# Kernel tuning notes

Measured on AMD Instinct MI355X. Metric: run time of the kernel, lower is better.

## Reference

```python
import jax, jax.numpy as jnp
import numpy as np
import math

B, N, E = 32, 512, 8192          # graphs, nodes/graph, edges/graph
IN_DIM, D, H, HD, L, C = 64, 128, 4, 32, 3, 10
HID = 2 * D                      # _FeatureMLP hidden = max(d, 2*d)


def _ln(x, g, b, eps=1e-5):
    mu = x.mean(-1, keepdims=True)
    var = ((x - mu) ** 2).mean(-1, keepdims=True)
    return (x - mu) / jnp.sqrt(var + eps) * g + b


def _gelu(x):
    return jax.nn.gelu(x, approximate=False)  # torch nn.GELU default (erf)


def setup_inputs() -> dict:
    key = jax.random.key(0)
    ks = iter(jax.random.split(key, 48))
    def w(*shape):
        return jax.random.normal(next(ks), shape, jnp.float32) * 0.02
    z = lambda *s: jnp.zeros(s, jnp.float32)
    o = lambda *s: jnp.ones(s, jnp.float32)
    return {
        'x': jax.random.normal(next(ks), (B * N, IN_DIM), jnp.float32),
        'src': jax.random.randint(next(ks), (B, E), 0, N),
        'dst': jax.random.randint(next(ks), (B, E), 0, N),
        # node encoder: Linear -> LN -> GELU -> Linear -> LN
        'enc_w1': w(IN_DIM, HID), 'enc_b1': z(HID), 'enc_g1': o(HID), 'enc_bn1': z(HID),
        'enc_w2': w(HID, D), 'enc_b2': z(D), 'enc_g2': o(D), 'enc_bn2': z(D),
        # per-layer edge-message MLP (stacked over L)
        'msg_w1': w(L, 2 * D, D), 'msg_b1': z(L, D),
        'msg_w2': w(L, D, D), 'msg_b2': z(L, D),
        'msg_g': o(L, D), 'msg_bb': z(L, D),
        # per-layer attention
        'qw': w(L, D, H * HD), 'qb': z(L, H * HD),
        'kw': w(L, D, H * HD), 'kb': z(L, H * HD),
        'vw': w(L, D, H * HD), 'vb': z(L, H * HD),
        'ow': w(L, H * HD, D), 'ob': z(L, D),
        'attn_g': o(L, D), 'attn_b': z(L, D),
        # graph head: Linear(4d,2d) -> GELU -> LN -> Linear(2d,C)
        'gh_w1': w(4 * D, 2 * D), 'gh_b1': z(2 * D),
        'gh_g': o(2 * D), 'gh_bn': z(2 * D),
        'gh_w2': w(2 * D, C), 'gh_b2': z(C),
    }


def reference(x, src, dst, enc_w1, enc_b1, enc_g1, enc_bn1, enc_w2, enc_b2, enc_g2, enc_bn2,
              msg_w1, msg_b1, msg_w2, msg_b2, msg_g, msg_bb,
              qw, qb, kw, kb, vw, vb, ow, ob, attn_g, attn_b,
              gh_w1, gh_b1, gh_g, gh_bn, gh_w2, gh_b2):
    # node encoder
    t = _ln(x @ enc_w1 + enc_b1, enc_g1, enc_bn1)
    h = _ln(_gelu(t) @ enc_w2 + enc_b2, enc_g2, enc_bn2)
    h = h.reshape(B, N, D)
    seg = jax.vmap(lambda m, d: jax.ops.segment_sum(m, d, num_segments=N))
    for l in range(L):
        # edge message block: gather src/dst, MLP, scatter-add to dst
        hs = jnp.take_along_axis(h, src[..., None], axis=1)   # [B,E,D]
        hd = jnp.take_along_axis(h, dst[..., None], axis=1)   # [B,E,D]
        m = _gelu(jnp.concatenate([hs, hd], -1) @ msg_w1[l] + msg_b1[l]) @ msg_w2[l] + msg_b2[l]
        h = _ln(h + seg(m, dst), msg_g[l], msg_bb[l])
        # masked attention block (dense per-graph attention)
        q = (h @ qw[l] + qb[l]).reshape(B, N, H, HD)
        k = (h @ kw[l] + kb[l]).reshape(B, N, H, HD)
        v = (h @ vw[l] + vb[l]).reshape(B, N, H, HD)
        scores = jnp.einsum('bnhd,bmhd->bhnm', q, k) / math.sqrt(HD)
        attn = jax.nn.softmax(scores, axis=-1)
        o = jnp.einsum('bhnm,bmhd->bnhd', attn, v).reshape(B, N, H * HD)
        h = _ln(h + o @ ow[l] + ob[l], attn_g[l], attn_b[l])
    # graph pooling: mean | sum | max | std
    mean = h.mean(1)
    summ = h.sum(1)
    mx = h.max(1)
    std = jnp.sqrt(jax.nn.relu((h ** 2).mean(1) - mean ** 2) + 1e-6)
    pool = jnp.concatenate([mean, summ, mx, std], -1)         # [B,4D]
    g = _ln(_gelu(pool @ gh_w1 + gh_b1), gh_g, gh_bn)
    return g @ gh_w2 + gh_b2                                   # [B,C]
```

## Files before the change

kernel.cpp:

```cpp
#include <hip/hip_runtime.h>
#include <cmath>

#define B_   32
#define N_   512
#define E_   8192
#define BN_  16384
#define D_   128

typedef short bf16x8 __attribute__((ext_vector_type(8)));
typedef float f32x4  __attribute__((ext_vector_type(4)));

static __device__ __forceinline__ float bf2f(unsigned short u){
  union{unsigned int i; float f;} v; v.i = ((unsigned int)u)<<16; return v.f;
}
static __device__ __forceinline__ unsigned short f2bf(float f){
  union{unsigned int i; float f;} v; v.f=f;
  unsigned int x=v.i;
  return (unsigned short)((x + 0x7fffu + ((x>>16)&1u))>>16);
}
static __device__ __forceinline__ unsigned int pack2(float a, float b){
  return (unsigned int)f2bf(a) | ((unsigned int)f2bf(b)<<16);
}
static __device__ __forceinline__ float gelu_f(float x){
  float xs=x*0.70710678118654752f;
  float ax=fabsf(xs);
  float t=__builtin_amdgcn_rcpf(1.0f+0.3275911f*ax);
  float p=t*(0.254829592f+t*(-0.284496736f+t*(1.421413741f+t*(-1.453152027f+t*1.061405429f))));
  float er=1.0f - p*__expf(-ax*ax);
  er = (xs<0.f)? -er : er;
  return 0.5f*x*(1.0f+er);
}
static __device__ __forceinline__ float gelu_t(float x){
  float x2=x*x;
  float y=x*(-1.5957691216f + x2*(-0.0713548162f));
  float e=__expf(y);
  return x*__builtin_amdgcn_rcpf(1.0f+e);
}
static __device__ __forceinline__ float ldin(const void* p, size_t i, int isbf){
  return isbf ? bf2f(((const unsigned short*)p)[i]) : ((const float*)p)[i];
}

static __device__ __forceinline__ void block_sum2(float a, float b, float&A, float&Bv, float* red, int nw){
  int lane=threadIdx.x&63, w=threadIdx.x>>6;
  #pragma unroll
  for(int o=32;o>0;o>>=1){ a+=__shfl_down(a,o); b+=__shfl_down(b,o); }
  if(lane==0){ red[w]=a; red[8+w]=b; }
  __syncthreads();
  float sa=0.f, sb=0.f;
  for(int i=0;i<nw;i++){ sa+=red[i]; sb+=red[8+i]; }
  __syncthreads();
  A=sa; Bv=sb;
}

__global__ void sniff_kernel(const unsigned int* __restrict__ xw, int* __restrict__ flag){
  int t=threadIdx.x;
  int cnt=0;
  for(int i=0;i<32;i++){
    unsigned int w=xw[t+64*i];
    float v=bf2f((unsigned short)(w&0xffffu));
    float av=fabsf(v);
    if(v==0.0f || (av>=6e-5f && av<=8.0f)) cnt++;
  }
  #pragma unroll
  for(int o=32;o>0;o>>=1) cnt+=__shfl_down(cnt,o);
  if(t==0) *flag=(cnt>=1024)?1:0;
}

__global__ __launch_bounds__(256) void count_kernel(
  const int* __restrict__ dst, int* __restrict__ cnt)
{
  __shared__ int lc[512];
  int g=blockIdx.x, c=blockIdx.y, t=threadIdx.x;
  for(int i=t;i<512;i+=256) lc[i]=0;
  __syncthreads();
  for(int e=t;e<1024;e+=256) atomicAdd(&lc[dst[(size_t)g*E_+c*1024+e]],1);
  __syncthreads();
  for(int i=t;i<512;i+=256){ int v=lc[i]; if(v) atomicAdd(&cnt[g*512+i],v); }
}

__global__ __launch_bounds__(256) void scan_kernel(
  int* __restrict__ cnt, int* __restrict__ rowptr)
{
  __shared__ int sc[512];
  int g=blockIdx.x, t=threadIdx.x;
  for(int i=t;i<512;i+=256) sc[i]=cnt[g*512+i];
  __syncthreads();
  if(t==0){
    int acc=0;
    for(int i=0;i<512;i++){ int c=sc[i]; rowptr[g*513+i]=acc; cnt[g*512+i]=acc; acc+=c; }
    rowptr[g*513+512]=acc;
  }
}

__global__ __launch_bounds__(256) void scatter_kernel(
  const int* __restrict__ src, const int* __restrict__ dst,
  int* __restrict__ off, unsigned short* __restrict__ ss)
{
  int g=blockIdx.x, c=blockIdx.y, t=threadIdx.x;
  for(int e=t;e<1024;e+=256){
    size_t idx=(size_t)g*E_+c*1024+e;
    int d=dst[idx];
    int pos=atomicAdd(&off[g*512+d],1);
    ss[(size_t)g*E_+pos]=(unsigned short)src[idx];
  }
}

__global__ __launch_bounds__(256) void prep_kernel(
  const void* __restrict__ msg_w1, const void* __restrict__ msg_w2,
  const void* __restrict__ qw, const void* __restrict__ kw,
  const void* __restrict__ vw, const void* __restrict__ ow,
  const void* __restrict__ qb, const void* __restrict__ kb, const void* __restrict__ vb,
  const void* __restrict__ ob, const void* __restrict__ msg_b1, const void* __restrict__ msg_b2,
  const void* __restrict__ msg_g, const void* __restrict__ msg_bb,
  const void* __restrict__ attn_g, const void* __restrict__ attn_b,
  const void* __restrict__ enc_w1, const void* __restrict__ enc_w2,
  const void* __restrict__ enc_b1, const void* __restrict__ enc_g1, const void* __restrict__ enc_bn1,
  const void* __restrict__ enc_b2, const void* __restrict__ enc_g2, const void* __restrict__ enc_bn2,
  const void* __restrict__ gh_w1, const void* __restrict__ gh_w2,
  const void* __restrict__ gh_b1, const void* __restrict__ gh_g,
  const void* __restrict__ gh_bn, const void* __restrict__ gh_b2,
  unsigned short* __restrict__ w1t, unsigned short* __restrict__ w2k,
  unsigned short* __restrict__ qkvt, unsigned short* __restrict__ owt,
  unsigned short* __restrict__ w1te, unsigned short* __restrict__ w2te,
  unsigned short* __restrict__ ghw1t, unsigned short* __restrict__ ghw2t,
  unsigned short* __restrict__ cb, const int* __restrict__ flag)
{
  int isbf=*flag;
  int job=blockIdx.y;
  int i=blockIdx.x*256+threadIdx.x;
  if(job<3){
    if(i<32768){ int l=job; int k=i>>7, n=i&127; w1t[l*32768 + n*256 + k]=f2bf(ldin(msg_w1,(size_t)l*32768+i,isbf)); }
  } else if(job<6){
    int l=job-3; if(i<16384){ w2k[l*16384 + i]=f2bf(ldin(msg_w2,(size_t)l*16384+i,isbf)); }
  } else if(job<15){
    int r=job-6, l=r/3, which=r%3;
    if(i<16384){ int k=i>>7, n=i&127;
      const void* w=(which==0)?qw:((which==1)?kw:vw);
      qkvt[l*49152 + (which*128+n)*128 + k]=f2bf(ldin(w,(size_t)l*16384+i,isbf)); }
  } else if(job<18){
    int l=job-15; if(i<16384){ int k=i>>7, n=i&127; owt[l*16384 + n*128 + k]=f2bf(ldin(ow,(size_t)l*16384+i,isbf)); }
  } else if(job==18){
    if(i<3840){
      float v;
      if(i<1152){ int l=i/384, j=i%384, which=j>>7, jj=j&127;
        const void* bb=(which==0)?qb:((which==1)?kb:vb);
        v=ldin(bb,(size_t)l*128+jj,isbf);
      } else {
        int i2=i-1152; int r=i2/384; int rem=i2%384;
        const void* s = (r==0)?ob:((r==1)?msg_b1:((r==2)?msg_b2:((r==3)?msg_g:((r==4)?msg_bb:((r==5)?attn_g:attn_b)))));
        v=ldin(s,(size_t)rem,isbf);
      }
      cb[i]=f2bf(v);
    }
  } else if(job==19){
    if(i<1152){
      float v;
      if(i<256)       v=ldin(enc_b1,i,isbf);
      else if(i<512)  v=ldin(enc_g1,i-256,isbf);
      else if(i<768)  v=ldin(enc_bn1,i-512,isbf);
      else if(i<896)  v=ldin(enc_b2,i-768,isbf);
      else if(i<1024) v=ldin(enc_g2,i-896,isbf);
      else            v=ldin(enc_bn2,i-1024,isbf);
      cb[3840+i]=f2bf(v);
    }
  } else if(job==20){
    if(i<16384){ int k=i>>8, n=i&255; w1te[n*64+k]=f2bf(ldin(enc_w1,(size_t)i,isbf)); }
  } else if(job==21){
    if(i<32768){ int k=i>>7, n=i&127; w2te[n*256+k]=f2bf(ldin(enc_w2,(size_t)i,isbf)); }
  } else if(job<26){
    int p=job-22; int j=p*32768+i;
    if(i<32768){ int k=j>>8, n=j&255; ghw1t[n*512+k]=f2bf(ldin(gh_w1,(size_t)j,isbf)); }
  } else {
    if(i<2560){ int k=i/10, n=i%10; ghw2t[n*256+k]=f2bf(ldin(gh_w2,(size_t)i,isbf)); }
    else if(i<2560+778){
      int j=i-2560; float v;
      if(j<256)      v=ldin(gh_b1,j,isbf);
      else if(j<512) v=ldin(gh_g,j-256,isbf);
      else if(j<768) v=ldin(gh_bn,j-512,isbf);
      else           v=ldin(gh_b2,j-768,isbf);
      cb[4992+j]=f2bf(v);
    }
  }
}

__global__ __launch_bounds__(256) void enc_kernel(
  const void* __restrict__ x, const unsigned short* __restrict__ w1te,
  const unsigned short* __restrict__ w2te, const unsigned short* __restrict__ cb,
  unsigned short* __restrict__ h, const int* __restrict__ flag)
{
  __shared__ __align__(16) unsigned short xs[64][72];
  __shared__ __align__(16) unsigned short t1[64][264];
  int isbf=*flag;
  int m0=blockIdx.x*64;
  int t=threadIdx.x, lane=t&63, w=t>>6, quad=lane>>4, ln=lane&15;
  for(int c2=t;c2<1024;c2+=256){
    int i=c2*4, row=i>>6, col=i&63;
    float v0,v1,v2,v3;
    if(isbf){
      const unsigned short* p=(const unsigned short*)x+(size_t)m0*64+i;
      v0=bf2f(p[0]); v1=bf2f(p[1]); v2=bf2f(p[2]); v3=bf2f(p[3]);
    } else {
      float4 f=*(const float4*)((const float*)x+(size_t)m0*64+i);
      v0=f.x; v1=f.y; v2=f.z; v3=f.w;
    }
    ushort4 o; o.x=f2bf(v0); o.y=f2bf(v1); o.z=f2bf(v2); o.w=f2bf(v3);
    *(ushort4*)&xs[row][col]=o;
  }
  __syncthreads();
  f32x4 a[4][4];
  #pragma unroll
  for(int nt=0;nt<4;nt++){ a[nt][0]={0,0,0,0}; a[nt][1]={0,0,0,0}; a[nt][2]={0,0,0,0}; a[nt][3]={0,0,0,0}; }
  #pragma unroll
  for(int k0i=0;k0i<2;k0i++){
    bf16x8 af[4];
    #pragma unroll
    for(int f=0;f<4;f++) af[f]=*(const bf16x8*)(&xs[f*16+ln][k0i*32+quad*8]);
    #pragma unroll
    for(int nt=0;nt<4;nt++){
      int n=w*64+nt*16+ln;
      bf16x8 bfr=*(const bf16x8*)(w1te+(size_t)n*64+k0i*32+quad*8);
      #pragma unroll
      for(int f=0;f<4;f++) a[nt][f]=__builtin_amdgcn_mfma_f32_16x16x32_bf16(af[f],bfr,a[nt][f],0,0,0);
    }
  }
  #pragma unroll
  for(int nt=0;nt<4;nt++){
    int n=w*64+nt*16+ln;
    float bv=bf2f(cb[3840+n]);
    #pragma unroll
    for(int f=0;f<4;f++)
      #pragma unroll
      for(int r=0;r<4;r++) t1[f*16+quad*4+r][n]=f2bf(a[nt][f][r]+bv);
  }
  __syncthreads();
  {
    int row=t>>2, qq=t&3;
    float s=0.f,s2=0.f;
    for(int c=qq*64;c<qq*64+64;c++){ float v=bf2f(t1[row][c]); s+=v; s2+=v*v; }
    s+=__shfl_xor(s,1); s+=__shfl_xor(s,2);
    s2+=__shfl_xor(s2,1); s2+=__shfl_xor(s2,2);
    float mu=s*(1.f/256.f), var=fmaxf(s2*(1.f/256.f)-mu*mu,0.f);
    float rr=rsqrtf(var+1e-5f);
    for(int c=qq*64;c<qq*64+64;c++){
      float v=bf2f(t1[row][c]);
      t1[row][c]=f2bf(gelu_f((v-mu)*rr*bf2f(cb[4096+c])+bf2f(cb[4352+c])));
    }
  }
  __syncthreads();
  f32x4 b2a[2][4];
  #pragma unroll
  for(int nt=0;nt<2;nt++){ b2a[nt][0]={0,0,0,0}; b2a[nt][1]={0,0,0,0}; b2a[nt][2]={0,0,0,0}; b2a[nt][3]={0,0,0,0}; }
  #pragma unroll
  for(int k0i=0;k0i<8;k0i++){
    bf16x8 af[4];
    #pragma unroll
    for(int f=0;f<4;f++) af[f]=*(const bf16x8*)(&t1[f*16+ln][k0i*32+quad*8]);
    #pragma unroll
    for(int nt=0;nt<2;nt++){
      int n=w*32+nt*16+ln;
      bf16x8 bfr=*(const bf16x8*)(w2te+(size_t)n*256+k0i*32+quad*8);
      #pragma unroll
      for(int f=0;f<4;f++) b2a[nt][f]=__builtin_amdgcn_mfma_f32_16x16x32_bf16(af[f],bfr,b2a[nt][f],0,0,0);
    }
  }
  __syncthreads();
  float* mf=(float*)&t1[0][0];
  #pragma unroll
  for(int nt=0;nt<2;nt++){
    int n=w*32+nt*16+ln;
    float bv=bf2f(cb[4608+n]);
    #pragma unroll
    for(int f=0;f<4;f++)
      #pragma unroll
      for(int r=0;r<4;r++) mf[(f*16+quad*4+r)*132+n]=b2a[nt][f][r]+bv;
  }
  __syncthreads();
  {
    int row=t>>2, qq=t&3;
    float s=0.f,s2=0.f;
    for(int c=qq*32;c<qq*32+32;c++){ float v=mf[row*132+c]; s+=v; s2+=v*v; }
    s+=__shfl_xor(s,1); s+=__shfl_xor(s,2);
    s2+=__shfl_xor(s2,1); s2+=__shfl_xor(s2,2);
    float mu=s*(1.f/128.f), var=fmaxf(s2*(1.f/128.f)-mu*mu,0.f);
    float rr=rsqrtf(var+1e-5f);
    for(int c=qq*32;c<qq*32+32;c+=2){
      float v0=(mf[row*132+c  ]-mu)*rr*bf2f(cb[4736+c  ])+bf2f(cb[4864+c  ]);
      float v1=(mf[row*132+c+1]-mu)*rr*bf2f(cb[4736+c+1])+bf2f(cb[4864+c+1]);
      *(unsigned int*)(h+(size_t)(m0+row)*128+c)=pack2(v0,v1);
    }
  }
}

__global__ __launch_bounds__(256) void uvgen_kernel(
  const unsigned short* __restrict__ hrows, const unsigned short* __restrict__ w1t,
  const unsigned short* __restrict__ b1, unsigned short* __restrict__ UV)
{
  __shared__ __align__(16) unsigned short a_t[64][136];
  int t=threadIdx.x;
  int m0=blockIdx.x*64;
  int y=blockIdx.y;
  for(int c=t;c<1024;c+=256){
    int m=c>>4, pp=c&15;
    *(uint4*)&a_t[m][pp*8]=*((const uint4*)(hrows+(size_t)(m0+m)*128)+pp);
  }
  __syncthreads();
  int lane=t&63, w=t>>6, quad=lane>>4, ln=lane&15;
  #pragma unroll
  for(int nt=0;nt<2;nt++){
    int n=w*32+nt*16+ln;
    f32x4 a0={0,0,0,0},a1={0,0,0,0},a2={0,0,0,0},a3={0,0,0,0};
    const unsigned short* wp=w1t+(size_t)n*256+y*128+quad*8;
    #pragma unroll
    for(int k0=0;k0<128;k0+=32){
      bf16x8 bfr=*(const bf16x8*)(wp+k0);
      bf16x8 f0=*(const bf16x8*)(&a_t[ln   ][k0+quad*8]);
      bf16x8 f1=*(const bf16x8*)(&a_t[16+ln][k0+quad*8]);
      bf16x8 f2=*(const bf16x8*)(&a_t[32+ln][k0+quad*8]);
      bf16x8 f3=*(const bf16x8*)(&a_t[48+ln][k0+quad*8]);
      a0=__builtin_amdgcn_mfma_f32_16x16x32_bf16(f0,bfr,a0,0,0,0);
      a1=__builtin_amdgcn_mfma_f32_16x16x32_bf16(f1,bfr,a1,0,0,0);
      a2=__builtin_amdgcn_mfma_f32_16x16x32_bf16(f2,bfr,a2,0,0,0);
      a3=__builtin_amdgcn_mfma_f32_16x16x32_bf16(f3,bfr,a3,0,0,0);
    }
    float bv=y?0.f:bf2f(b1[n]);
    #pragma unroll
    for(int r2=0;r2<4;r2++){
      UV[(size_t)(m0+quad*4+r2   )*256+y*128+n]=f2bf(a0[r2]+bv);
      UV[(size_t)(m0+16+quad*4+r2)*256+y*128+n]=f2bf(a1[r2]+bv);
      UV[(size_t)(m0+32+quad*4+r2)*256+y*128+n]=f2bf(a2[r2]+bv);
      UV[(size_t)(m0+48+quad*4+r2)*256+y*128+n]=f2bf(a3[r2]+bv);
    }
  }
}

__global__ __launch_bounds__(128) void edgef_kernel(
  unsigned short* __restrict__ h,
  const unsigned short* __restrict__ UV,
  const unsigned short* __restrict__ ss,
  const int* __restrict__ rowptr,
  const unsigned short* __restrict__ w2k,
  const unsigned short* __restrict__ b2,
  const unsigned short* __restrict__ gg, const unsigned short* __restrict__ bbp,
  int b0, int gEp)
{
  __shared__ __align__(16) float aggL[2][4][128];
  __shared__ __align__(16) float po[2][4][128];
  int t=threadIdx.x, lane=t&63, w=t>>6;
  int bid=blockIdx.x;
  int lg=bid%gEp, ch=bid/gEp;
  int g=b0+lg;
  const unsigned short* UVg = UV + (size_t)lg*512*256;
  const unsigned short* ssg = ss + (size_t)g*E_;
  int dbase = ch*4;
  int bnd[5];
  #pragma unroll
  for(int i=0;i<5;i++) bnd[i]=rowptr[g*513+dbase+i];
  #pragma unroll 1
  for(int dd=0;dd<4;dd++){
    int e_lo=bnd[dd], e_hi0=bnd[dd+1];
    int half=(e_hi0-e_lo+1)>>1;
    int es = w ? (e_lo+half) : e_lo;
    int ee = w ? e_hi0       : (e_lo+half);
    unsigned int vdw=*(const unsigned int*)(UVg + (size_t)(dbase+dd)*256 + 128 + lane*2);
    float v0=bf2f((unsigned short)(vdw&0xffffu)), v1=bf2f((unsigned short)(vdw>>16));
    float a0=0.f, a1=0.f;
    int si3,si4,si5;
    unsigned int u0,u1,u2;
    {
      int s0=__builtin_amdgcn_readfirstlane((int)ssg[es  ])&511;
      int s1=__builtin_amdgcn_readfirstlane((int)ssg[es+1])&511;
      int s2=__builtin_amdgcn_readfirstlane((int)ssg[es+2])&511;
      si3=(int)ssg[es+3]; si4=(int)ssg[es+4]; si5=(int)ssg[es+5];
      u0=*(const unsigned int*)(UVg + (size_t)s0*256 + lane*2);
      u1=*(const unsigned int*)(UVg + (size_t)s1*256 + lane*2);
      u2=*(const unsigned int*)(UVg + (size_t)s2*256 + lane*2);
    }
    #pragma unroll 2
    for(int e=es;e<ee;e++){
      float z0=bf2f((unsigned short)(u0&0xffffu))+v0;
      float z1=bf2f((unsigned short)(u0>>16))+v1;
      u0=u1; u1=u2;
      int s3=__builtin_amdgcn_readfirstlane(si3)&511;
      u2=*(const unsigned int*)(UVg + (size_t)s3*256 + lane*2);
      si3=si4; si4=si5;
      si5=(int)ssg[e+6];
      a0+=gelu_t(z0); a1+=gelu_t(z1);
    }
    aggL[w][dd][lane*2  ]=a0;
    aggL[w][dd][lane*2+1]=a1;
  }
  __syncthreads();
  float o[4][2];
  #pragma unroll
  for(int dd=0;dd<4;dd++){ o[dd][0]=0.f; o[dd][1]=0.f; }
  #pragma unroll 4
  for(int kk=0;kk<64;kk++){
    int k=w*64+kk;
    unsigned int wdw=*(const unsigned int*)(w2k+(size_t)k*128+lane*2);
    float w0=bf2f((unsigned short)(wdw&0xffffu));
    float w1=bf2f((unsigned short)(wdw>>16));
    #pragma unroll
    for(int dd=0;dd<4;dd++){
      float av=aggL[0][dd][k]+aggL[1][dd][k];
      o[dd][0]+=av*w0; o[dd][1]+=av*w1;
    }
  }
  #pragma unroll
  for(int dd=0;dd<4;dd++){
    po[w][dd][lane*2  ]=o[dd][0];
    po[w][dd][lane*2+1]=o[dd][1];
  }
  __syncthreads();
  #pragma unroll 1
  for(int p=0;p<2;p++){
    int di=w*2+p;
    int d = dbase + di;
    float deg=(float)(bnd[di+1]-bnd[di]);
    float o0=bf2f(b2[lane*2  ])*deg + po[0][di][lane*2  ] + po[1][di][lane*2  ];
    float o1=bf2f(b2[lane*2+1])*deg + po[0][di][lane*2+1] + po[1][di][lane*2+1];
    size_t base=(size_t)(g*512+d)*128;
    unsigned int hdw=*(const unsigned int*)(h+base+lane*2);
    float x0=bf2f((unsigned short)(hdw&0xffffu))+o0;
    float x1=bf2f((unsigned short)(hdw>>16))+o1;
    float s1=x0+x1, s2=x0*x0+x1*x1;
    #pragma unroll
    for(int off=32;off>0;off>>=1){ s1+=__shfl_xor(s1,off); s2+=__shfl_xor(s2,off); }
    float mu=s1*(1.f/128.f), var=fmaxf(s2*(1.f/128.f)-mu*mu,0.f);
    float rr=rsqrtf(var+1e-5f);
    float y0=(x0-mu)*rr*bf2f(gg[lane*2  ])+bf2f(bbp[lane*2  ]);
    float y1=(x1-mu)*rr*bf2f(gg[lane*2+1])+bf2f(bbp[lane*2+1]);
    *(unsigned int*)(h+base+lane*2)=pack2(y0,y1);
  }
}

__global__ __launch_bounds__(256) void attnf_kernel(
  const unsigned short* __restrict__ h, const unsigned short* __restrict__ wqkv,
  const unsigned short* __restrict__ bq, unsigned short* __restrict__ obuf, int b0, int gA)
{
  __shared__ __align__(16) unsigned short Qs[128][40];
  __shared__ __align__(16) unsigned short Ks[64][72];
  __shared__ __align__(16) unsigned short Vts[32][72];
  __shared__ __align__(16) unsigned short Ps[64][72];
  int bx=blockIdx.x;
  int lg=bx%gA; int rr2=bx/gA; int hh=rr2&3, qq4=rr2>>2;
  int g=b0+lg;
  int t=threadIdx.x, lane=t&63, w=t>>6, quad=lane>>4, ln=lane&15;
  const unsigned short* hg=h+(size_t)g*512*128;
  const float sc=0.17677669529663689f;
  bf16x8 wk[2][4], wv[2][4];
  #pragma unroll
  for(int nt=0;nt<2;nt++)
    #pragma unroll
    for(int k0i=0;k0i<4;k0i++){
      int n=hh*32+nt*16+ln;
      wk[nt][k0i]=*(const bf16x8*)(wqkv+(size_t)(128+n)*128+k0i*32+quad*8);
      wv[nt][k0i]=*(const bf16x8*)(wqkv+(size_t)(256+n)*128+k0i*32+quad*8);
    }
  #pragma unroll
  for(int qt=0;qt<2;qt++){
    int r0=qq4*128+qt*64+w*16;
    bf16x8 af[4];
    #pragma unroll
    for(int k0i=0;k0i<4;k0i++) af[k0i]=*(const bf16x8*)(hg+(size_t)(r0+ln)*128+k0i*32+quad*8);
    #pragma unroll
    for(int nt=0;nt<2;nt++){
      int dim=nt*16+ln;
      f32x4 c={0,0,0,0};
      #pragma unroll
      for(int k0i=0;k0i<4;k0i++){
        bf16x8 bfr=*(const bf16x8*)(wqkv+(size_t)(hh*32+dim)*128+k0i*32+quad*8);
        c=__builtin_amdgcn_mfma_f32_16x16x32_bf16(af[k0i],bfr,c,0,0,0);
      }
      float bv=bf2f(bq[hh*32+dim]);
      #pragma unroll
      for(int r=0;r<4;r++) Qs[qt*64+w*16+quad*4+r][dim]=f2bf((c[r]+bv)*sc);
    }
  }
  f32x4 O[2][2]; float Lp[2][4];
  #pragma unroll
  for(int qt=0;qt<2;qt++){ O[qt][0]={0,0,0,0}; O[qt][1]={0,0,0,0};
    #pragma unroll
    for(int r=0;r<4;r++) Lp[qt][r]=0.f; }
  for(int kc=0;kc<8;kc++){
    __syncthreads();
    {
      int r0=kc*64+w*16;
      bf16x8 af[4];
      #pragma unroll
      for(int k0i=0;k0i<4;k0i++) af[k0i]=*(const bf16x8*)(hg+(size_t)(r0+ln)*128+k0i*32+quad*8);
      #pragma unroll
      for(int nt=0;nt<2;nt++){
        int dim=nt*16+ln;
        f32x4 ck={0,0,0,0}, cv={0,0,0,0};
        #pragma unroll
        for(int k0i=0;k0i<4;k0i++){
          ck=__builtin_amdgcn_mfma_f32_16x16x32_bf16(af[k0i],wk[nt][k0i],ck,0,0,0);
          cv=__builtin_amdgcn_mfma_f32_16x16x32_bf16(af[k0i],wv[nt][k0i],cv,0,0,0);
        }
        float bk=bf2f(bq[128+hh*32+dim]), bv2=bf2f(bq[256+hh*32+dim]);
        #pragma unroll
        for(int r=0;r<4;r++){
          int key=w*16+quad*4+r;
          Ks[key][dim]=f2bf(ck[r]+bk);
          Vts[dim][key]=f2bf(cv[r]+bv2);
        }
      }
    }
    __syncthreads();
    #pragma unroll
    for(int qt=0;qt<2;qt++){
      bf16x8 qf=*(const bf16x8*)(&Qs[qt*64+w*16+ln][quad*8]);
      f32x4 s[4];
      #pragma unroll
      for(int f=0;f<4;f++){
        bf16x8 kf=*(const bf16x8*)(&Ks[f*16+ln][quad*8]);
        f32x4 z={0,0,0,0};
        s[f]=__builtin_amdgcn_mfma_f32_16x16x32_bf16(qf,kf,z,0,0,0);
      }
      #pragma unroll
      for(int f=0;f<4;f++)
        #pragma unroll
        for(int r=0;r<4;r++){
          float pe=__expf(fminf(s[f][r],30.0f));
          Ps[w*16+quad*4+r][f*16+ln]=f2bf(pe);
          Lp[qt][r]+=pe;
        }
      #pragma unroll
      for(int s2=0;s2<2;s2++){
        bf16x8 pf=*(const bf16x8*)(&Ps[w*16+ln][s2*32+quad*8]);
        bf16x8 v0=*(const bf16x8*)(&Vts[ln   ][s2*32+quad*8]);
        bf16x8 v1=*(const bf16x8*)(&Vts[16+ln][s2*32+quad*8]);
        O[qt][0]=__builtin_amdgcn_mfma_f32_16x16x32_bf16(pf,v0,O[qt][0],0,0,0);
        O[qt][1]=__builtin_amdgcn_mfma_f32_16x16x32_bf16(pf,v1,O[qt][1],0,0,0);
      }
    }
  }
  #pragma unroll
  for(int qt=0;qt<2;qt++){
    #pragma unroll
    for(int o=1;o<16;o<<=1)
      #pragma unroll
      for(int r=0;r<4;r++) Lp[qt][r]+=__shfl_xor(Lp[qt][r],o);
    #pragma unroll
    for(int r=0;r<4;r++){
      float inv=1.0f/Lp[qt][r];
      size_t row=(size_t)lg*512+qq4*128+qt*64+w*16+quad*4+r;
      obuf[row*128+hh*32+ln   ]=f2bf(O[qt][0][r]*inv);
      obuf[row*128+hh*32+16+ln]=f2bf(O[qt][1][r]*inv);
    }
  }
}

__global__ __launch_bounds__(256) void oproj_kernel(
  const unsigned short* __restrict__ obuf, const unsigned short* __restrict__ wo,
  const unsigned short* __restrict__ bo, unsigned short* __restrict__ h,
  const unsigned short* __restrict__ gg, const unsigned short* __restrict__ bbp, int b0)
{
  __shared__ __align__(16) unsigned short a_t[64][136];
  __shared__ float mf[64][132];
  int t=threadIdx.x, lane=t&63, w=t>>6, quad=lane>>4, ln=lane&15;
  int m0=blockIdx.x*64;
  for(int c=t;c<64*16;c+=256){
    int m=c>>4, pp=c&15;
    *(uint4*)&a_t[m][pp*8]=*((const uint4*)(obuf+(size_t)(m0+m)*128)+pp);
  }
  __syncthreads();
  #pragma unroll
  for(int nt=0;nt<2;nt++){
    int n=w*32+nt*16+ln;
    f32x4 a0={0,0,0,0},a1={0,0,0,0},a2={0,0,0,0},a3={0,0,0,0};
    const unsigned short* wp=wo+(size_t)n*128+quad*8;
    #pragma unroll
    for(int k0=0;k0<128;k0+=32){
      bf16x8 bfr=*(const bf16x8*)(wp+k0);
      bf16x8 f0=*(const bf16x8*)(&a_t[ln   ][k0+quad*8]);
      bf16x8 f1=*(const bf16x8*)(&a_t[16+ln][k0+quad*8]);
      bf16x8 f2=*(const bf16x8*)(&a_t[32+ln][k0+quad*8]);
      bf16x8 f3=*(const bf16x8*)(&a_t[48+ln][k0+quad*8]);
      a0=__builtin_amdgcn_mfma_f32_16x16x32_bf16(f0,bfr,a0,0,0,0);
      a1=__builtin_amdgcn_mfma_f32_16x16x32_bf16(f1,bfr,a1,0,0,0);
      a2=__builtin_amdgcn_mfma_f32_16x16x32_bf16(f2,bfr,a2,0,0,0);
      a3=__builtin_amdgcn_mfma_f32_16x16x32_bf16(f3,bfr,a3,0,0,0);
    }
    float bv=bf2f(bo[n]);
    #pragma unroll
    for(int r=0;r<4;r++){
      mf[quad*4+r   ][n]=a0[r]+bv;
      mf[16+quad*4+r][n]=a1[r]+bv;
      mf[32+quad*4+r][n]=a2[r]+bv;
      mf[48+quad*4+r][n]=a3[r]+bv;
    }
  }
  __syncthreads();
  {
    int row=t>>2, qq=t&3;
    size_t base=(size_t)(b0*512+m0+row)*128;
    float s=0.f,s2=0.f;
    float vals[32];
    for(int j=0;j<32;j++){
      int c=qq*32+j;
      float v=bf2f(h[base+c])+mf[row][c];
      vals[j]=v; s+=v; s2+=v*v;
    }
    s+=__shfl_xor(s,1); s+=__shfl_xor(s,2);
    s2+=__shfl_xor(s2,1); s2+=__shfl_xor(s2,2);
    float mu=s*(1.f/128.f), var=fmaxf(s2*(1.f/128.f)-mu*mu,0.f);
    float rr=rsqrtf(var+1e-5f);
    for(int j=0;j<32;j+=2){
      int c=qq*32+j;
      float v0=(vals[j]  -mu)*rr*bf2f(gg[c  ])+bf2f(bbp[c  ]);
      float v1=(vals[j+1]-mu)*rr*bf2f(gg[c+1])+bf2f(bbp[c+1]);
      *(unsigned int*)(h+base+c)=pack2(v0,v1);
    }
  }
}

__global__ __launch_bounds__(256) void poolp_kernel(
  const unsigned short* __restrict__ h, float* __restrict__ part)
{
  __shared__ float ps[256], ps2[256], pm[256];
  int b=blockIdx.x, c=blockIdx.y;
  int t=threadIdx.x, d=t&127, hf=t>>7;
  float s=0.f,s2=0.f,mx=-1e30f;
  for(int r=hf*32;r<hf*32+32;r++){
    float v=bf2f(h[((size_t)(b*512+c*64+r))*128+d]);
    s+=v; s2+=v*v; mx=fmaxf(mx,v);
  }
  ps[t]=s; ps2[t]=s2; pm[t]=mx;
  __syncthreads();
  if(t<128){
    s=ps[t]+ps[128+t]; s2=ps2[t]+ps2[128+t]; mx=fmaxf(pm[t],pm[128+t]);
    size_t base=((size_t)(b*8+c))*384;
    part[base+t]=s; part[base+128+t]=s2; part[base+256+t]=mx;
  }
}

__global__ __launch_bounds__(256) void head_kernel(
  const float* __restrict__ part, const unsigned short* __restrict__ ghw1t,
  const unsigned short* __restrict__ ghw2t, const unsigned short* __restrict__ cb,
  void* __restrict__ out, const int* __restrict__ flag)
{
  int isbf=*flag;
  int b=blockIdx.x, t=threadIdx.x;
  __shared__ float pl[512];
  __shared__ float gl[256];
  __shared__ float red[16];
  if(t<128){
    float s=0.f,s2=0.f,mx=-1e30f;
    for(int c=0;c<8;c++){
      size_t base=((size_t)(b*8+c))*384;
      s += part[base+t];
      s2+= part[base+128+t];
      mx = fmaxf(mx, part[base+256+t]);
    }
    float mean=s*(1.f/512.f);
    float var=fmaxf(s2*(1.f/512.f)-mean*mean,0.f);
    float sd=sqrtf(var+1e-6f);
    pl[t]=mean; pl[128+t]=s; pl[256+t]=mx; pl[384+t]=sd;
  }
  __syncthreads();
  float a=bf2f(cb[4992+t]);
  const unsigned short* wr=ghw1t+(size_t)t*512;
  for(int k0=0;k0<512;k0+=8){
    bf16x8 wv=*(const bf16x8*)(wr+k0);
    const unsigned short* wp=(const unsigned short*)&wv;
    #pragma unroll
    for(int j=0;j<8;j++) a+=pl[k0+j]*bf2f(wp[j]);
  }
  float u=gelu_f(a);
  float S,S2; block_sum2(u,u*u,S,S2,red,4);
  float mu=S*(1.f/256.f), var=fmaxf(S2*(1.f/256.f)-mu*mu,0.f);
  float r=rsqrtf(var+1e-5f);
  gl[t]=(u-mu)*r*bf2f(cb[5248+t])+bf2f(cb[5504+t]);
  __syncthreads();
  if(t<10){
    float o=bf2f(cb[5760+t]);
    const unsigned short* wr2=ghw2t+(size_t)t*256;
    for(int k0=0;k0<256;k0+=8){
      bf16x8 wv=*(const bf16x8*)(wr2+k0);
      const unsigned short* wp=(const unsigned short*)&wv;
      #pragma unroll
      for(int j=0;j<8;j++) o+=gl[k0+j]*bf2f(wp[j]);
    }
    if(isbf) ((unsigned short*)out)[b*10+t]=f2bf(o);
    else     ((float*)out)[b*10+t]=o;
  }
}

extern "C" void kernel_launch(void* const* d_in, const int* in_sizes, int n_in,
                              void* d_out, int out_size, void* d_ws, size_t ws_size,
                              hipStream_t stream)
{
  const void* x      =d_in[0];
  const int*  src    =(const int*)d_in[1];
  const int*  dstp   =(const int*)d_in[2];
  const void* enc_w1 =d_in[3];  const void* enc_b1 =d_in[4];
  const void* enc_g1 =d_in[5];  const void* enc_bn1=d_in[6];
  const void* enc_w2 =d_in[7];  const void* enc_b2 =d_in[8];
  const void* enc_g2 =d_in[9];  const void* enc_bn2=d_in[10];
  const void* msg_w1 =d_in[11]; const void* msg_b1 =d_in[12];
  const void* msg_w2 =d_in[13]; const void* msg_b2 =d_in[14];
  const void* msg_g  =d_in[15]; const void* msg_bb =d_in[16];
  const void* qw     =d_in[17]; const void* qb     =d_in[18];
  const void* kw     =d_in[19]; const void* kb     =d_in[20];
  const void* vw     =d_in[21]; const void* vb     =d_in[22];
  const void* ow     =d_in[23]; const void* ob     =d_in[24];
  const void* attn_g =d_in[25]; const void* attn_b =d_in[26];
  const void* gh_w1  =d_in[27]; const void* gh_b1  =d_in[28];
  const void* gh_g   =d_in[29]; const void* gh_bn  =d_in[30];
  const void* gh_w2  =d_in[31]; const void* gh_b2  =d_in[32];
  (void)in_sizes; (void)n_in; (void)out_size;

  const size_t MB=1024*1024;
  char* base=(char*)d_ws;
  unsigned short* h    =(unsigned short*)(base);
  unsigned short* w1t  =(unsigned short*)(base + 4194304);
  unsigned short* w2k  =(unsigned short*)(base + 4390912);
  unsigned short* qkvt =(unsigned short*)(base + 4489216);
  unsigned short* owt  =(unsigned short*)(base + 4784128);
  unsigned short* w1te =(unsigned short*)(base + 4882432);
  unsigned short* w2te =(unsigned short*)(base + 4915200);
  unsigned short* ghw1t=(unsigned short*)(base + 4980736);
  unsigned short* ghw2t=(unsigned short*)(base + 5242880);
  unsigned short* cb   =(unsigned short*)(base + 5248000);
  int*   rowptr        =(int*)(base + 5325312);
  int*   flag          =(int*)(base + 5390976);
  int*   cnt           =(int*)(base + 5391360);
  unsigned short* ssrt =(unsigned short*)(base + 5505024);
  char* R              = base + 6029312;

  int epass, apass;
  if(ws_size >= (size_t)(14.5*MB)){ epass=1; apass=1; }
  else if(ws_size >= 10*MB){ epass=2; apass=1; }
  else { epass=4; apass=2; }
  int gEp=B_/epass, gA=B_/apass;
  int rowsA=gA*512;
  float* part=(float*)R;

  sniff_kernel<<<1,64,0,stream>>>((const unsigned int*)x, flag);
  hipMemsetAsync(cnt,0,65536,stream);
  count_kernel<<<dim3(B_,8),256,0,stream>>>(dstp,cnt);
  scan_kernel<<<B_,256,0,stream>>>(cnt,rowptr);
  scatter_kernel<<<dim3(B_,8),256,0,stream>>>(src,dstp,cnt,ssrt);
  prep_kernel<<<dim3(128,27),256,0,stream>>>(msg_w1,msg_w2,qw,kw,vw,ow,qb,kb,vb,
      ob,msg_b1,msg_b2,msg_g,msg_bb,attn_g,attn_b,
      enc_w1,enc_w2,enc_b1,enc_g1,enc_bn1,enc_b2,enc_g2,enc_bn2,
      gh_w1,gh_w2,gh_b1,gh_g,gh_bn,gh_b2,
      w1t,w2k,qkvt,owt,w1te,w2te,ghw1t,ghw2t,cb,flag);

  enc_kernel<<<BN_/64,256,0,stream>>>(x,w1te,w2te,cb,h,flag);

  for(int l=0;l<3;l++){
    for(int ep=0;ep<epass;ep++){
      int b0=ep*gEp;
      unsigned short* UV=(unsigned short*)R;
      uvgen_kernel<<<dim3(gEp*8,2),256,0,stream>>>(h+(size_t)b0*512*128,
          w1t+(size_t)l*32768, cb+1536+l*128, UV);
      edgef_kernel<<<gEp*128,128,0,stream>>>(h,UV,ssrt,rowptr,
          w2k+(size_t)l*16384, cb+1920+l*128, cb+2304+l*128, cb+2688+l*128, b0, gEp);
    }
    for(int ap=0;ap<apass;ap++){
      int b0=ap*gA;
      unsigned short* obuf=(unsigned short*)R;
      attnf_kernel<<<gA*16,256,0,stream>>>(h, qkvt+(size_t)l*49152, cb+l*384, obuf, b0, gA);
      oproj_kernel<<<rowsA/64,256,0,stream>>>(obuf, owt+(size_t)l*16384,
          cb+1152+l*128, h, cb+3072+l*128, cb+3456+l*128, b0);
    }
  }
  poolp_kernel<<<dim3(B_,8),256,0,stream>>>(h,part);
  head_kernel<<<B_,256,0,stream>>>(part,ghw1t,ghw2t,cb,d_out,flag);
}
```

Baseline: 436.9 us.

## Precompute Q/K/V in separate GEMM kernel instead of recomputing inside attention

Adds a qkvgen kernel that computes Q (pre-scaled), K, and a transposed V for all nodes once per layer and writes them to workspace. The attention kernel then loads K and V fragments directly from global memory instead of recomputing the K/V projections in every block (each of the 4 query-tiles per head previously recomputed K/V for all 512 keys). This also removes the LDS staging and two barriers per key chunk. In exchange it adds a kernel launch and extra global traffic for Q/K/V, and the workspace split into passes now depends on available capacity.

```diff
diff --git a/kernel.cpp b/kernel.cpp
--- a/kernel.cpp
+++ b/kernel.cpp
@@ -333,6 +333,73 @@
   }
 }
 
+__global__ __launch_bounds__(256) void qkvgen_kernel(
+  const unsigned short* __restrict__ hrows, const unsigned short* __restrict__ wqkv,
+  const unsigned short* __restrict__ bqkv,
+  unsigned short* __restrict__ Qb, unsigned short* __restrict__ Kb,
+  unsigned short* __restrict__ Vtb)
+{
+  __shared__ __align__(16) unsigned short a_t[64][136];
+  int t=threadIdx.x;
+  int m0=blockIdx.x*64;
+  int y=blockIdx.y;
+  for(int c=t;c<1024;c+=256){
+    int m=c>>4, pp=c&15;
+    *(uint4*)&a_t[m][pp*8]=*((const uint4*)(hrows+(size_t)(m0+m)*128)+pp);
+  }
+  __syncthreads();
+  int lane=t&63, w=t>>6, quad=lane>>4, ln=lane&15;
+  int gloc=m0>>9, r0=m0&511;
+  #pragma unroll
+  for(int nt=0;nt<2;nt++){
+    int n=w*32+nt*16+ln;
+    f32x4 a0={0,0,0,0},a1={0,0,0,0},a2={0,0,0,0},a3={0,0,0,0};
+    const unsigned short* wp=wqkv+(size_t)(y*128+n)*128+quad*8;
+    #pragma unroll
+    for(int k0=0;k0<128;k0+=32){
+      bf16x8 bfr=*(const bf16x8*)(wp+k0);
+      bf16x8 f0=*(const bf16x8*)(&a_t[ln   ][k0+quad*8]);
+      bf16x8 f1=*(const bf16x8*)(&a_t[16+ln][k0+quad*8]);
+      bf16x8 f2=*(const bf16x8*)(&a_t[32+ln][k0+quad*8]);
+      bf16x8 f3=*(const bf16x8*)(&a_t[48+ln][k0+quad*8]);
+      a0=__builtin_amdgcn_mfma_f32_16x16x32_bf16(f0,bfr,a0,0,0,0);
+      a1=__builtin_amdgcn_mfma_f32_16x16x32_bf16(f1,bfr,a1,0,0,0);
+      a2=__builtin_amdgcn_mfma_f32_16x16x32_bf16(f2,bfr,a2,0,0,0);
+      a3=__builtin_amdgcn_mfma_f32_16x16x32_bf16(f3,bfr,a3,0,0,0);
+    }
+    float bv=bf2f(bqkv[y*128+n]);
+    if(y==0){
+      const float sc=0.17677669529663689f;
+      #pragma unroll
+      for(int r=0;r<4;r++){
+        Qb[(size_t)(m0   +quad*4+r)*128+n]=f2bf((a0[r]+bv)*sc);
+        Qb[(size_t)(m0+16+quad*4+r)*128+n]=f2bf((a1[r]+bv)*sc);
+        Qb[(size_t)(m0+32+quad*4+r)*128+n]=f2bf((a2[r]+bv)*sc);
+        Qb[(size_t)(m0+48+quad*4+r)*128+n]=f2bf((a3[r]+bv)*sc);
+      }
+    } else if(y==1){
+      #pragma unroll
+      for(int r=0;r<4;r++){
+        Kb[(size_t)(m0   +quad*4+r)*128+n]=f2bf(a0[r]+bv);
+        Kb[(size_t)(m0+16+quad*4+r)*128+n]=f2bf(a1[r]+bv);
+        Kb[(size_t)(m0+32+quad*4+r)*128+n]=f2bf(a2[r]+bv);
+        Kb[(size_t)(m0+48+quad*4+r)*128+n]=f2bf(a3[r]+bv);
+      }
+    } else {
+      unsigned short* vrow = Vtb + ((size_t)gloc*128+n)*512 + r0 + quad*4;
+      ushort4 o;
+      o.x=f2bf(a0[0]+bv); o.y=f2bf(a0[1]+bv); o.z=f2bf(a0[2]+bv); o.w=f2bf(a0[3]+bv);
+      *(ushort4*)(vrow)=o;
+      o.x=f2bf(a1[0]+bv); o.y=f2bf(a1[1]+bv); o.z=f2bf(a1[2]+bv); o.w=f2bf(a1[3]+bv);
+      *(ushort4*)(vrow+16)=o;
+      o.x=f2bf(a2[0]+bv); o.y=f2bf(a2[1]+bv); o.z=f2bf(a2[2]+bv); o.w=f2bf(a2[3]+bv);
+      *(ushort4*)(vrow+32)=o;
+      o.x=f2bf(a3[0]+bv); o.y=f2bf(a3[1]+bv); o.z=f2bf(a3[2]+bv); o.w=f2bf(a3[3]+bv);
+      *(ushort4*)(vrow+48)=o;
+    }
+  }
+}
+
 __global__ __launch_bounds__(128) void edgef_kernel(
   unsigned short* __restrict__ h,
   const unsigned short* __restrict__ UV,
@@ -434,88 +501,41 @@
 }
 
 __global__ __launch_bounds__(256) void attnf_kernel(
-  const unsigned short* __restrict__ h, const unsigned short* __restrict__ wqkv,
-  const unsigned short* __restrict__ bq, unsigned short* __restrict__ obuf, int b0, int gA)
-{
-  __shared__ __align__(16) unsigned short Qs[128][40];
-  __shared__ __align__(16) unsigned short Ks[64][72];
-  __shared__ __align__(16) unsigned short Vts[32][72];
+  const unsigned short* __restrict__ Qb, const unsigned short* __restrict__ Kb,
+  const unsigned short* __restrict__ Vtb, unsigned short* __restrict__ obuf, int gA)
+{
   __shared__ __align__(16) unsigned short Ps[64][72];
   int bx=blockIdx.x;
   int lg=bx%gA; int rr2=bx/gA; int hh=rr2&3, qq4=rr2>>2;
-  int g=b0+lg;
   int t=threadIdx.x, lane=t&63, w=t>>6, quad=lane>>4, ln=lane&15;
-  const unsigned short* hg=h+(size_t)g*512*128;
-  const float sc=0.17677669529663689f;
-  bf16x8 wk[2][4], wv[2][4];
-  #pragma unroll
-  for(int nt=0;nt<2;nt++)
-    #pragma unroll
-    for(int k0i=0;k0i<4;k0i++){
-      int n=hh*32+nt*16+ln;
-      wk[nt][k0i]=*(const bf16x8*)(wqkv+(size_t)(128+n)*128+k0i*32+quad*8);
-      wv[nt][k0i]=*(const bf16x8*)(wqkv+(size_t)(256+n)*128+k0i*32+quad*8);
-    }
-  #pragma unroll
-  for(int qt=0;qt<2;qt++){
-    int r0=qq4*128+qt*64+w*16;
-    bf16x8 af[4];
-    #pragma unroll
-    for(int k0i=0;k0i<4;k0i++) af[k0i]=*(const bf16x8*)(hg+(size_t)(r0+ln)*128+k0i*32+quad*8);
-    #pragma unroll
-    for(int nt=0;nt<2;nt++){
-      int dim=nt*16+ln;
-      f32x4 c={0,0,0,0};
-      #pragma unroll
-      for(int k0i=0;k0i<4;k0i++){
-        bf16x8 bfr=*(const bf16x8*)(wqkv+(size_t)(hh*32+dim)*128+k0i*32+quad*8);
-        c=__builtin_amdgcn_mfma_f32_16x16x32_bf16(af[k0i],bfr,c,0,0,0);
-      }
-      float bv=bf2f(bq[hh*32+dim]);
-      #pragma unroll
-      for(int r=0;r<4;r++) Qs[qt*64+w*16+quad*4+r][dim]=f2bf((c[r]+bv)*sc);
-    }
-  }
+  const unsigned short* Kg = Kb + (size_t)lg*65536 + hh*32;
+  const unsigned short* Vg = Vtb + ((size_t)lg*128+hh*32)*512;
+  bf16x8 qf[2];
+  #pragma unroll
+  for(int qt=0;qt<2;qt++)
+    qf[qt]=*(const bf16x8*)(Qb + (size_t)(lg*512+qq4*128+qt*64+w*16+ln)*128 + hh*32 + quad*8);
   f32x4 O[2][2]; float Lp[2][4];
   #pragma unroll
   for(int qt=0;qt<2;qt++){ O[qt][0]={0,0,0,0}; O[qt][1]={0,0,0,0};
     #pragma unroll
     for(int r=0;r<4;r++) Lp[qt][r]=0.f; }
   for(int kc=0;kc<8;kc++){
-    __syncthreads();
-    {
-      int r0=kc*64+w*16;
-      bf16x8 af[4];
-      #pragma unroll
-      for(int k0i=0;k0i<4;k0i++) af[k0i]=*(const bf16x8*)(hg+(size_t)(r0+ln)*128+k0i*32+quad*8);
-      #pragma unroll
-      for(int nt=0;nt<2;nt++){
-        int dim=nt*16+ln;
-        f32x4 ck={0,0,0,0}, cv={0,0,0,0};
-        #pragma unroll
-        for(int k0i=0;k0i<4;k0i++){
-          ck=__builtin_amdgcn_mfma_f32_16x16x32_bf16(af[k0i],wk[nt][k0i],ck,0,0,0);
-          cv=__builtin_amdgcn_mfma_f32_16x16x32_bf16(af[k0i],wv[nt][k0i],cv,0,0,0);
-        }
-        float bk=bf2f(bq[128+hh*32+dim]), bv2=bf2f(bq[256+hh*32+dim]);
-        #pragma unroll
-        for(int r=0;r<4;r++){
-          int key=w*16+quad*4+r;
-          Ks[key][dim]=f2bf(ck[r]+bk);
-          Vts[dim][key]=f2bf(cv[r]+bv2);
-        }
-      }
-    }
-    __syncthreads();
+    bf16x8 kf[4];
+    #pragma unroll
+    for(int f=0;f<4;f++) kf[f]=*(const bf16x8*)(Kg + (size_t)(kc*64+f*16+ln)*128 + quad*8);
+    bf16x8 va[2], vb[2];
+    #pragma unroll
+    for(int s2=0;s2<2;s2++){
+      va[s2]=*(const bf16x8*)(Vg + (size_t)ln*512      + kc*64 + s2*32 + quad*8);
+      vb[s2]=*(const bf16x8*)(Vg + (size_t)(16+ln)*512 + kc*64 + s2*32 + quad*8);
+    }
     #pragma unroll
     for(int qt=0;qt<2;qt++){
-      bf16x8 qf=*(const bf16x8*)(&Qs[qt*64+w*16+ln][quad*8]);
       f32x4 s[4];
       #pragma unroll
       for(int f=0;f<4;f++){
-        bf16x8 kf=*(const bf16x8*)(&Ks[f*16+ln][quad*8]);
         f32x4 z={0,0,0,0};
-        s[f]=__builtin_amdgcn_mfma_f32_16x16x32_bf16(qf,kf,z,0,0,0);
+        s[f]=__builtin_amdgcn_mfma_f32_16x16x32_bf16(qf[qt],kf[f],z,0,0,0);
       }
       #pragma unroll
       for(int f=0;f<4;f++)
@@ -528,10 +548,8 @@
       #pragma unroll
       for(int s2=0;s2<2;s2++){
         bf16x8 pf=*(const bf16x8*)(&Ps[w*16+ln][s2*32+quad*8]);
-        bf16x8 v0=*(const bf16x8*)(&Vts[ln   ][s2*32+quad*8]);
-        bf16x8 v1=*(const bf16x8*)(&Vts[16+ln][s2*32+quad*8]);
-        O[qt][0]=__builtin_amdgcn_mfma_f32_16x16x32_bf16(pf,v0,O[qt][0],0,0,0);
-        O[qt][1]=__builtin_amdgcn_mfma_f32_16x16x32_bf16(pf,v1,O[qt][1],0,0,0);
+        O[qt][0]=__builtin_amdgcn_mfma_f32_16x16x32_bf16(pf,va[s2],O[qt][0],0,0,0);
+        O[qt][1]=__builtin_amdgcn_mfma_f32_16x16x32_bf16(pf,vb[s2],O[qt][1],0,0,0);
       }
     }
   }
@@ -711,7 +729,6 @@
   const void* gh_w2  =d_in[31]; const void* gh_b2  =d_in[32];
   (void)in_sizes; (void)n_in; (void)out_size;
 
-  const size_t MB=1024*1024;
   char* base=(char*)d_ws;
   unsigned short* h    =(unsigned short*)(base);
   unsigned short* w1t  =(unsigned short*)(base + 4194304);
@@ -729,12 +746,10 @@
   unsigned short* ssrt =(unsigned short*)(base + 5505024);
   char* R              = base + 6029312;
 
-  int epass, apass;
-  if(ws_size >= (size_t)(14.5*MB)){ epass=1; apass=1; }
-  else if(ws_size >= 10*MB){ epass=2; apass=1; }
-  else { epass=4; apass=2; }
-  int gEp=B_/epass, gA=B_/apass;
-  int rowsA=gA*512;
+  size_t Rcap = (ws_size > 6029312) ? (ws_size - 6029312) : 0;
+  int gA = 32;  while(gA  > 4 && (size_t)gA *524288 > Rcap) gA  >>= 1;
+  int gEp= 32;  while(gEp > 4 && (size_t)gEp*262144 > Rcap) gEp >>= 1;
+  int epass = 32/gEp, apass = 32/gA;
   float* part=(float*)R;
 
   sniff_kernel<<<1,64,0,stream>>>((const unsigned int*)x, flag);
@@ -761,9 +776,14 @@
     }
     for(int ap=0;ap<apass;ap++){
       int b0=ap*gA;
-      unsigned short* obuf=(unsigned short*)R;
-      attnf_kernel<<<gA*16,256,0,stream>>>(h, qkvt+(size_t)l*49152, cb+l*384, obuf, b0, gA);
-      oproj_kernel<<<rowsA/64,256,0,stream>>>(obuf, owt+(size_t)l*16384,
+      unsigned short* Qb  =(unsigned short*)R;
+      unsigned short* Kb  =Qb  + (size_t)gA*65536;
+      unsigned short* Vtb =Kb  + (size_t)gA*65536;
+      unsigned short* obuf=Vtb + (size_t)gA*65536;
+      qkvgen_kernel<<<dim3(gA*8,3),256,0,stream>>>(h+(size_t)b0*512*128,
+          qkvt+(size_t)l*49152, cb+l*384, Qb, Kb, Vtb);
+      attnf_kernel<<<gA*16,256,0,stream>>>(Qb, Kb, Vtb, obuf, gA);
+      oproj_kernel<<<gA*8,256,0,stream>>>(obuf, owt+(size_t)l*16384,
           cb+1152+l*128, h, cb+3072+l*128, cb+3456+l*128, b0);
     }
   }
```

Measured after the change: 426.8 us. -2.3%, faster.
